# Kernel tuning notes

Measured on AMD Instinct MI355X. Metric: run time of the kernel, lower is better.

## Reference

```python
import jax, jax.numpy as jnp
import numpy as np


def setup_inputs() -> dict:
    key = jax.random.key(0)
    k1, k2, k3 = jax.random.split(key, 3)
    T, B, D, H = 256, 64, 1024, 2048
    sigma = 0.01
    inputs = jax.random.normal(k1, (T, B, D), dtype=jnp.float32)
    state = jnp.zeros((B, H), dtype=jnp.float32)
    W_xh = jax.random.uniform(k2, (D, H), dtype=jnp.float32) * sigma
    W_hh = jax.random.uniform(k3, (H, H), dtype=jnp.float32) * sigma
    b_h = jnp.zeros((H,), dtype=jnp.float32)
    return {"inputs": inputs, "state": state, "W_xh": W_xh, "W_hh": W_hh, "b_h": b_h}


def reference(inputs, state, W_xh, W_hh, b_h):
    # Precompute input projection for all steps in one big GEMM: [T,B,H]
    x_proj = jnp.einsum('tbd,dh->tbh', inputs, W_xh) + b_h

    def step(h, xp):
        h = jnp.tanh(h @ W_hh + xp)
        return h, h

    final_state, outputs = jax.lax.scan(step, state, x_proj)
    # outputs: [T, B, H] (stacked per-step hidden states), final_state: [B, H]
    return outputs, final_state
```

## Files before the change

### kernel.cpp

```cpp
#include <hip/hip_runtime.h>
#include <hip/hip_bf16.h>

#define T_STEPS 256
#define B_SZ    64
#define D_SZ    1024
#define H_SZ    2048
#define NBLK    256
#define TPB     320
#define HBUF    (B_SZ * H_SZ)

#define W_SCALE     256.0f
#define W_INV_SCALE 0.00390625f

typedef __attribute__((ext_vector_type(8))) _Float16 f16x8;
typedef __attribute__((ext_vector_type(4))) _Float16 f16x4;
typedef __attribute__((ext_vector_type(4))) float    f32x4;


__global__ void cvt_f32_f16(const float* __restrict__ in,
                            _Float16* __restrict__ out, int n4, float scale) {
    int i = blockIdx.x * blockDim.x + threadIdx.x;
    if (i < n4) {
        float4 v = ((const float4*)in)[i];
        f16x4 o = { (_Float16)(v.x * scale), (_Float16)(v.y * scale),
                    (_Float16)(v.z * scale), (_Float16)(v.w * scale) };
        ((f16x4*)out)[i] = o;
    }
}

__global__ void transpose_to_f16(const float* __restrict__ in,
                                 _Float16* __restrict__ out,
                                 int rows, int cols, float scale) {
    __shared__ float tile[32][33];
    int tx = threadIdx.x & 31, ty = threadIdx.x >> 5;
    int r0 = blockIdx.y * 32, c0 = blockIdx.x * 32;
#pragma unroll
    for (int i = 0; i < 32; i += 8)
        tile[ty + i][tx] = in[(size_t)(r0 + ty + i) * cols + c0 + tx];
    __syncthreads();
#pragma unroll
    for (int i = 0; i < 32; i += 8)
        out[(size_t)(c0 + ty + i) * rows + r0 + tx] = (_Float16)(tile[tx][ty + i] * scale);
}

__global__ void init_ctrs(unsigned int* ctr) {
    ctr[threadIdx.x + blockIdx.x * blockDim.x] = 0u;
}

#define GBK 32
__device__ __forceinline__ void gload_lds16(const _Float16* g, _Float16* l) {
    __builtin_amdgcn_global_load_lds((const __attribute__((address_space(1))) void*)g,
                                     (__attribute__((address_space(3))) void*)l, 16, 0, 0);
}

__global__ __launch_bounds__(256) void gemm_xproj(
    const _Float16* __restrict__ A,
    const _Float16* __restrict__ BT,
    const float* __restrict__ bias,
    float* __restrict__ C,
    int M, int N, int K)
{
    __shared__ _Float16 As[128 * GBK];
    __shared__ _Float16 Bs[128 * GBK];

    int tid  = threadIdx.x;
    int wave = tid >> 6;
    int lane = tid & 63;
    int q = lane >> 4;
    int r = lane & 15;
    int m0 = blockIdx.x * 128;
    int n0 = blockIdx.y * 128;
    int wr = (wave >> 1) * 64;
    int wc = (wave & 1) * 64;

    int srow  = lane >> 2;
    int skoff = (lane & 3) * 8;

    f32x4 acc[4][4] = {};
    for (int k0 = 0; k0 < K; k0 += GBK) {
#pragma unroll
        for (int i = 0; i < 2; i++) {
            int chunk = wave * 2 + i;
            int row = chunk * 16 + srow;
            gload_lds16(A  + (size_t)(m0 + row) * K + k0 + skoff, As + chunk * 512);
            gload_lds16(BT + (size_t)(n0 + row) * K + k0 + skoff, Bs + chunk * 512);
        }
        __asm__ volatile("s_waitcnt vmcnt(0)" ::: "memory");
        __syncthreads();

        f16x8 a[4], b[4];
#pragma unroll
        for (int i = 0; i < 4; i++)
            a[i] = *(const f16x8*)(As + (wr + i * 16 + r) * GBK + q * 8);
#pragma unroll
        for (int j = 0; j < 4; j++)
            b[j] = *(const f16x8*)(Bs + (wc + j * 16 + r) * GBK + q * 8);
#pragma unroll
        for (int i = 0; i < 4; i++)
#pragma unroll
            for (int j = 0; j < 4; j++)
                acc[i][j] = __builtin_amdgcn_mfma_f32_16x16x32_f16(a[i], b[j], acc[i][j], 0, 0, 0);
        __syncthreads();
    }
#pragma unroll
    for (int i = 0; i < 4; i++)
#pragma unroll
        for (int j = 0; j < 4; j++)
#pragma unroll
            for (int reg = 0; reg < 4; reg++) {
                int row = m0 + wr + i * 16 + q * 4 + reg;
                int col = n0 + wc + j * 16 + r;
                C[(size_t)row * N + col] = acc[i][j][reg] * W_INV_SCALE + bias[col];
            }
}

template<bool CHAIN>
__global__ __launch_bounds__(TPB, 1) void rnn_persist(
    _Float16* __restrict__ hbase,
    _Float16* __restrict__ hb1,
    const _Float16* __restrict__ WT,
    float* __restrict__ out,
    float* __restrict__ final_out,
    unsigned int* __restrict__ ctr)
{
    __shared__ f16x8 wfrag[8192];
    __shared__ float part[4][2][256];
    __shared__ __align__(16) _Float16 hsl[16 * 32];
    __shared__ int pdone[4];
    __shared__ int hdone1, go;

    int tid = threadIdx.x;
    int bid = blockIdx.x;
    int g   = (bid >> 1) & 3;
    int c   = ((bid >> 3) << 1) | (bid & 1);
    int n0  = c * 32;
    int row0 = g * 16;

    if (tid == 0) {
        pdone[0] = pdone[1] = pdone[2] = pdone[3] = 0;
        hdone1 = 0; go = 0;
    }

    for (int idx = tid; idx < 8192; idx += TPB) {
        int kb = idx >> 7, j = (idx >> 6) & 1, l = idx & 63;
        wfrag[idx] = *(const f16x8*)(WT + (size_t)(n0 + j * 16 + (l & 15)) * H_SZ
                                        + kb * 32 + (l >> 4) * 8);
    }
    __syncthreads();

    int wave = tid >> 6, lane = tid & 63;

    if (wave == 4) {
        float c0 = 1.0f + lane, c1 = 2.0f, c2 = 3.0f, c3 = 4.0f;
        const float k1 = 1.0000001f, k2 = 1.0e-30f;
        while (__hip_atomic_load(&go, __ATOMIC_RELAXED, __HIP_MEMORY_SCOPE_WORKGROUP) < T_STEPS) {
#pragma unroll
            for (int z = 0; z < 64; z++) {
                c0 = __builtin_fmaf(c0, k1, k2);
                c1 = __builtin_fmaf(c1, k1, k2);
                c2 = __builtin_fmaf(c2, k1, k2);
                c3 = __builtin_fmaf(c3, k1, k2);
            }
        }
        __asm__ volatile("" :: "v"(c0), "v"(c1), "v"(c2), "v"(c3));
        return;
    }

    int q = lane >> 4, r = lane & 15;
    unsigned int* aline = ctr + (g * 2 + (bid & 1)) * 32;

    float xp[4];
    if (wave < 2) {
#pragma unroll
        for (int s = 0; s < 4; s++)
            xp[s] = out[(size_t)(row0 + q + 4 * s) * H_SZ + n0 + wave * 16 + r];
    }

    for (int t = 0; t < T_STEPS; t++) {
        const _Float16* hp;
        _Float16*       hn;
        if constexpr (CHAIN) {
            hp = hbase + (size_t)t * HBUF;
            hn = hbase + (size_t)(t + 1) * HBUF;
        } else {
            hp = (t & 1) ? hb1 : hbase;
            hn = (t & 1) ? hbase : hb1;
        }
        float* out_t = out + (size_t)t * B_SZ * H_SZ;
        int tg = t + 1;

        const _Float16* arow = hp + (size_t)(row0 + r) * H_SZ + q * 8;
        f16x8 abuf[16];
#pragma unroll
        for (int p = 0; p < 16; p++) {
            if constexpr (CHAIN) {
                abuf[p] = *(const f16x8*)(arow + (wave * 16 + p) * 32);
            } else {
                union { unsigned long long u[2]; f16x8 v; } au;
                au.u[0] = __hip_atomic_load((unsigned long long*)(arow + (wave * 16 + p) * 32),
                                            __ATOMIC_RELAXED, __HIP_MEMORY_SCOPE_AGENT);
                au.u[1] = __hip_atomic_load((unsigned long long*)(arow + (wave * 16 + p) * 32) + 1,
                                            __ATOMIC_RELAXED, __HIP_MEMORY_SCOPE_AGENT);
                abuf[p] = au.v;
            }
        }
        f32x4 acc[2] = {};
#pragma unroll
        for (int p = 0; p < 16; p++) {
            int kb = wave * 16 + p;
            acc[0] = __builtin_amdgcn_mfma_f32_16x16x32_f16(abuf[p], wfrag[kb * 128 + lane],      acc[0], 0, 0, 0);
            acc[1] = __builtin_amdgcn_mfma_f32_16x16x32_f16(abuf[p], wfrag[kb * 128 + 64 + lane], acc[1], 0, 0, 0);
        }

#pragma unroll
        for (int h = 0; h < 2; h++)
            *(f32x4*)&part[wave][h][lane * 4] = acc[h];
        __asm__ volatile("s_waitcnt lgkmcnt(0)" ::: "memory");
        if (lane == 0)
            __hip_atomic_store(&pdone[wave], tg, __ATOMIC_RELAXED, __HIP_MEMORY_SCOPE_WORKGROUP);

        if (wave >= 2) {
            if (t == T_STEPS - 1) break;
            while (__hip_atomic_load(&go, __ATOMIC_RELAXED, __HIP_MEMORY_SCOPE_WORKGROUP) < tg) { }
            continue;
        }

        for (int w = 0; w < 4; w++)
            if (w != wave)
                while (__hip_atomic_load(&pdone[w], __ATOMIC_RELAXED, __HIP_MEMORY_SCOPE_WORKGROUP) < tg) { }
        __asm__ volatile("" ::: "memory");

        bool last = (t == T_STEPS - 1);
#pragma unroll
        for (int s = 0; s < 4; s++) {
            int row = q + 4 * s;
            int idx = (s * 16 + r) * 4 + q;
            float sum = part[0][wave][idx] + part[1][wave][idx]
                      + part[2][wave][idx] + part[3][wave][idx];
            float v = tanhf(sum * W_INV_SCALE + xp[s]);
            size_t o = (size_t)(row0 + row) * H_SZ + n0 + wave * 16 + r;
            out_t[o] = v;
            if (last) final_out[o] = v;
            hsl[row * 32 + wave * 16 + r] = (_Float16)v;
        }
        if (last) {
            if (wave == 0 && lane == 0)
                __hip_atomic_store(&go, T_STEPS, __ATOMIC_RELAXED, __HIP_MEMORY_SCOPE_WORKGROUP);
            break;
        }

        const float* out_t1 = out_t + B_SZ * H_SZ;
#pragma unroll
        for (int s = 0; s < 4; s++)
            xp[s] = out_t1[(size_t)(row0 + q + 4 * s) * H_SZ + n0 + wave * 16 + r];

        __asm__ volatile("s_waitcnt lgkmcnt(0)" ::: "memory");
        {
            int rl = lane >> 2, pi = wave * 4 + (lane & 3);
            unsigned long long vv = ((const unsigned long long*)hsl)[rl * 8 + pi];
            __hip_atomic_store((unsigned long long*)(hn + (size_t)(row0 + rl) * H_SZ + n0) + pi,
                               vv, __ATOMIC_RELAXED, __HIP_MEMORY_SCOPE_AGENT);
        }
        __builtin_amdgcn_s_waitcnt(0);

        if (wave == 1) {
            if (lane == 0)
                __hip_atomic_store(&hdone1, tg, __ATOMIC_RELAXED, __HIP_MEMORY_SCOPE_WORKGROUP);
            while (__hip_atomic_load(&go, __ATOMIC_RELAXED, __HIP_MEMORY_SCOPE_WORKGROUP) < tg) { }
            continue;
        }
        while (__hip_atomic_load(&hdone1, __ATOMIC_RELAXED, __HIP_MEMORY_SCOPE_WORKGROUP) < tg) { }
        if (lane == 0)
            __hip_atomic_fetch_add(aline, 1u, __ATOMIC_RELAXED, __HIP_MEMORY_SCOPE_AGENT);
        unsigned int line_tgt = (unsigned int)tg * 32u;
        for (;;) {
            unsigned int v = __hip_atomic_load(ctr + (g * 2 + (lane & 1)) * 32,
                                               __ATOMIC_RELAXED, __HIP_MEMORY_SCOPE_AGENT);
            if (__ballot(v < line_tgt) == 0ull) break;
        }
        if (lane == 0)
            __hip_atomic_store(&go, tg, __ATOMIC_RELAXED, __HIP_MEMORY_SCOPE_WORKGROUP);
    }
}


extern "C" void kernel_launch(void* const* d_in, const int* in_sizes, int n_in,
                              void* d_out, int out_size, void* d_ws, size_t ws_size,
                              hipStream_t stream) {
    const float* inputs = (const float*)d_in[0];
    const float* state  = (const float*)d_in[1];
    const float* W_xh   = (const float*)d_in[2];
    const float* W_hh   = (const float*)d_in[3];
    const float* b_h    = (const float*)d_in[4];
    float* out = (float*)d_out;
    char* ws = (char*)d_ws;

    const size_t MB = 1ull << 20;
    const size_t OFF_WXT   = 0;
    const size_t OFF_WHT   = 4 * MB;
    const size_t OFF_CTR   = 12 * MB;
    const size_t OFF_CHAIN = 12 * MB + 8192;
    const size_t NEED_CHAIN = OFF_CHAIN + (size_t)(T_STEPS + 1) * HBUF * 2;

    const size_t F_IN  = 0;
    const size_t F_WXT = F_IN  + (size_t)T_STEPS * B_SZ * D_SZ * 2;
    const size_t F_WHT = F_WXT + (size_t)H_SZ * D_SZ * 2;
    const size_t F_H0  = F_WHT + (size_t)H_SZ * H_SZ * 2;
    const size_t F_H1  = F_H0  + (size_t)HBUF * 2;
    const size_t F_CTR = F_H1  + (size_t)HBUF * 2;
    const size_t NEED_PP = F_CTR + 4096;

    const int n_in_el = T_STEPS * B_SZ * D_SZ;
    dim3 g1((T_STEPS * B_SZ) / 128, H_SZ / 128);
    float* final_out = out + (size_t)T_STEPS * B_SZ * H_SZ;

    if (ws_size >= NEED_CHAIN) {
        _Float16* WxT    = (_Float16*)(ws + OFF_WXT);
        _Float16* WhT    = (_Float16*)(ws + OFF_WHT);
        unsigned int* ctr = (unsigned int*)(ws + OFF_CTR);
        _Float16* hchain = (_Float16*)(ws + OFF_CHAIN);
        _Float16* inputs_f16 = hchain + HBUF;
        _Float16* hb1 = nullptr;

        cvt_f32_f16<<<(n_in_el / 4 + 255) / 256, 256, 0, stream>>>(inputs, inputs_f16, n_in_el / 4, 1.0f);
        transpose_to_f16<<<dim3(H_SZ / 32, D_SZ / 32), 256, 0, stream>>>(W_xh, WxT, D_SZ, H_SZ, W_SCALE);
        transpose_to_f16<<<dim3(H_SZ / 32, H_SZ / 32), 256, 0, stream>>>(W_hh, WhT, H_SZ, H_SZ, W_SCALE);
        cvt_f32_f16<<<(B_SZ * H_SZ / 4 + 255) / 256, 256, 0, stream>>>(state, hchain, B_SZ * H_SZ / 4, 1.0f);
        init_ctrs<<<4, 256, 0, stream>>>(ctr);

        gemm_xproj<<<g1, 256, 0, stream>>>(inputs_f16, WxT, b_h, out,
                                           T_STEPS * B_SZ, H_SZ, D_SZ);

        void* args[] = { (void*)&hchain, (void*)&hb1, (void*)&WhT,
                         (void*)&out, (void*)&final_out, (void*)&ctr };
        hipLaunchCooperativeKernel((void*)rnn_persist<true>, dim3(NBLK), dim3(TPB),
                                   args, 0, stream);
    } else {
        if (ws_size < NEED_PP) return;
        _Float16* inputs_f16 = (_Float16*)(ws + F_IN);
        _Float16* WxT    = (_Float16*)(ws + F_WXT);
        _Float16* WhT    = (_Float16*)(ws + F_WHT);
        _Float16* hbuf0  = (_Float16*)(ws + F_H0);
        _Float16* hbuf1  = (_Float16*)(ws + F_H1);
        unsigned int* ctr = (unsigned int*)(ws + F_CTR);

        cvt_f32_f16<<<(n_in_el / 4 + 255) / 256, 256, 0, stream>>>(inputs, inputs_f16, n_in_el / 4, 1.0f);
        transpose_to_f16<<<dim3(H_SZ / 32, D_SZ / 32), 256, 0, stream>>>(W_xh, WxT, D_SZ, H_SZ, W_SCALE);
        transpose_to_f16<<<dim3(H_SZ / 32, H_SZ / 32), 256, 0, stream>>>(W_hh, WhT, H_SZ, H_SZ, W_SCALE);
        cvt_f32_f16<<<(B_SZ * H_SZ / 4 + 255) / 256, 256, 0, stream>>>(state, hbuf0, B_SZ * H_SZ / 4, 1.0f);
        init_ctrs<<<4, 256, 0, stream>>>(ctr);

        gemm_xproj<<<g1, 256, 0, stream>>>(inputs_f16, WxT, b_h, out,
                                           T_STEPS * B_SZ, H_SZ, D_SZ);

        void* args[] = { (void*)&hbuf0, (void*)&hbuf1, (void*)&WhT,
                         (void*)&out, (void*)&final_out, (void*)&ctr };
        hipLaunchCooperativeKernel((void*)rnn_persist<false>, dim3(NBLK), dim3(TPB),
                                   args, 0, stream);
    }
}
```

Baseline: 1.654 ms.

## Replace group barrier with per-block step flags and fuse prep kernels

Replaces the per-step counter barrier across the 64 blocks of a batch group with per-block step flags. Each block publishes its own step count, and each consumer wave polls only the flags of the producer blocks whose columns it reads, so the global barrier and the 'go' broadcast are gone. A local pread handshake stops waves from overwriting the partial sums before they have been consumed. The five preprocessing launches are also merged into one prep_all kernel to save launch overhead. The risk is more flag polling traffic and subtle ordering bugs in the relaxed-memory handshake.

```diff
diff --git a/kernel.cpp b/kernel.cpp
--- a/kernel.cpp
+++ b/kernel.cpp
@@ -16,24 +16,17 @@
 typedef __attribute__((ext_vector_type(4))) _Float16 f16x4;
 typedef __attribute__((ext_vector_type(4))) float    f32x4;
 
-
-__global__ void cvt_f32_f16(const float* __restrict__ in,
-                            _Float16* __restrict__ out, int n4, float scale) {
-    int i = blockIdx.x * blockDim.x + threadIdx.x;
-    if (i < n4) {
-        float4 v = ((const float4*)in)[i];
-        f16x4 o = { (_Float16)(v.x * scale), (_Float16)(v.y * scale),
-                    (_Float16)(v.z * scale), (_Float16)(v.w * scale) };
-        ((f16x4*)out)[i] = o;
-    }
-}
-
-__global__ void transpose_to_f16(const float* __restrict__ in,
-                                 _Float16* __restrict__ out,
-                                 int rows, int cols, float scale) {
-    __shared__ float tile[32][33];
+#define PREP_NI   16384
+#define PREP_NTX  (64 * 32)
+#define PREP_NTH  (64 * 64)
+#define PREP_NS   128
+#define PREP_TOT  (PREP_NI + PREP_NTX + PREP_NTH + PREP_NS + 1)
+
+__device__ __forceinline__ void tile_transpose(
+    const float* __restrict__ in, _Float16* __restrict__ out,
+    int rows, int cols, int bx, int by, float scale, float (*tile)[33]) {
     int tx = threadIdx.x & 31, ty = threadIdx.x >> 5;
-    int r0 = blockIdx.y * 32, c0 = blockIdx.x * 32;
+    int r0 = by * 32, c0 = bx * 32;
 #pragma unroll
     for (int i = 0; i < 32; i += 8)
         tile[ty + i][tx] = in[(size_t)(r0 + ty + i) * cols + c0 + tx];
@@ -43,8 +36,34 @@
         out[(size_t)(c0 + ty + i) * rows + r0 + tx] = (_Float16)(tile[tx][ty + i] * scale);
 }
 
-__global__ void init_ctrs(unsigned int* ctr) {
-    ctr[threadIdx.x + blockIdx.x * blockDim.x] = 0u;
+__global__ void prep_all(const float* __restrict__ inputs, _Float16* __restrict__ xin,
+                         const float* __restrict__ W_xh, _Float16* __restrict__ WxT,
+                         const float* __restrict__ W_hh, _Float16* __restrict__ WhT,
+                         const float* __restrict__ state, _Float16* __restrict__ h0,
+                         unsigned int* __restrict__ ctr) {
+    __shared__ float tile[32][33];
+    int bid = blockIdx.x, tid = threadIdx.x;
+    if (bid < PREP_NI) {
+        int i = bid * 256 + tid;
+        float4 v = ((const float4*)inputs)[i];
+        f16x4 o = { (_Float16)v.x, (_Float16)v.y, (_Float16)v.z, (_Float16)v.w };
+        ((f16x4*)xin)[i] = o;
+    } else if (bid < PREP_NI + PREP_NTX) {
+        int rel = bid - PREP_NI;
+        tile_transpose(W_xh, WxT, D_SZ, H_SZ, rel % 64, rel / 64, W_SCALE, tile);
+    } else if (bid < PREP_NI + PREP_NTX + PREP_NTH) {
+        int rel = bid - PREP_NI - PREP_NTX;
+        tile_transpose(W_hh, WhT, H_SZ, H_SZ, rel % 64, rel / 64, W_SCALE, tile);
+    } else if (bid < PREP_NI + PREP_NTX + PREP_NTH + PREP_NS) {
+        int rel = bid - PREP_NI - PREP_NTX - PREP_NTH;
+        int i = rel * 256 + tid;
+        float4 v = ((const float4*)state)[i];
+        f16x4 o = { (_Float16)v.x, (_Float16)v.y, (_Float16)v.z, (_Float16)v.w };
+        ((f16x4*)h0)[i] = o;
+    } else {
+#pragma unroll
+        for (int k = 0; k < 4; k++) ctr[k * 256 + tid] = 0u;
+    }
 }
 
 #define GBK 32
@@ -127,6 +146,7 @@
     __shared__ float part[4][2][256];
     __shared__ __align__(16) _Float16 hsl[16 * 32];
     __shared__ int pdone[4];
+    __shared__ int pread[2];
     __shared__ int hdone1, go;
 
     int tid = threadIdx.x;
@@ -138,6 +158,7 @@
 
     if (tid == 0) {
         pdone[0] = pdone[1] = pdone[2] = pdone[3] = 0;
+        pread[0] = pread[1] = 0;
         hdone1 = 0; go = 0;
     }
 
@@ -167,7 +188,9 @@
     }
 
     int q = lane >> 4, r = lane & 15;
-    unsigned int* aline = ctr + (g * 2 + (bid & 1)) * 32;
+    unsigned int* flags = ctr + g * 64;
+    unsigned int* myflag = flags + c;
+    unsigned int* pflag  = flags + wave * 16 + (lane & 15);
 
     float xp[4];
     if (wave < 2) {
@@ -188,6 +211,16 @@
         }
         float* out_t = out + (size_t)t * B_SZ * H_SZ;
         int tg = t + 1;
+
+        if (t > 0) {
+            unsigned int need = (unsigned int)t;
+            for (;;) {
+                unsigned int v = __hip_atomic_load(pflag, __ATOMIC_RELAXED,
+                                                   __HIP_MEMORY_SCOPE_AGENT);
+                if (__ballot(v < need) == 0ull) break;
+            }
+            __asm__ volatile("" ::: "memory");
+        }
 
         const _Float16* arow = hp + (size_t)(row0 + r) * H_SZ + q * 8;
         f16x8 abuf[16];
@@ -212,6 +245,12 @@
             acc[1] = __builtin_amdgcn_mfma_f32_16x16x32_f16(abuf[p], wfrag[kb * 128 + 64 + lane], acc[1], 0, 0, 0);
         }
 
+        if (t > 0) {
+            while (__hip_atomic_load(&pread[0], __ATOMIC_RELAXED, __HIP_MEMORY_SCOPE_WORKGROUP) < t ||
+                   __hip_atomic_load(&pread[1], __ATOMIC_RELAXED, __HIP_MEMORY_SCOPE_WORKGROUP) < t) { }
+            __asm__ volatile("" ::: "memory");
+        }
+
 #pragma unroll
         for (int h = 0; h < 2; h++)
             *(f32x4*)&part[wave][h][lane * 4] = acc[h];
@@ -221,7 +260,6 @@
 
         if (wave >= 2) {
             if (t == T_STEPS - 1) break;
-            while (__hip_atomic_load(&go, __ATOMIC_RELAXED, __HIP_MEMORY_SCOPE_WORKGROUP) < tg) { }
             continue;
         }
 
@@ -231,13 +269,20 @@
         __asm__ volatile("" ::: "memory");
 
         bool last = (t == T_STEPS - 1);
+        float sums[4];
+#pragma unroll
+        for (int s = 0; s < 4; s++) {
+            int idx = (s * 16 + r) * 4 + q;
+            sums[s] = part[0][wave][idx] + part[1][wave][idx]
+                    + part[2][wave][idx] + part[3][wave][idx];
+        }
+        if (lane == 0)
+            __hip_atomic_store(&pread[wave], tg, __ATOMIC_RELAXED, __HIP_MEMORY_SCOPE_WORKGROUP);
+
 #pragma unroll
         for (int s = 0; s < 4; s++) {
             int row = q + 4 * s;
-            int idx = (s * 16 + r) * 4 + q;
-            float sum = part[0][wave][idx] + part[1][wave][idx]
-                      + part[2][wave][idx] + part[3][wave][idx];
-            float v = tanhf(sum * W_INV_SCALE + xp[s]);
+            float v = tanhf(sums[s] * W_INV_SCALE + xp[s]);
             size_t o = (size_t)(row0 + row) * H_SZ + n0 + wave * 16 + r;
             out_t[o] = v;
             if (last) final_out[o] = v;
@@ -266,20 +311,12 @@
         if (wave == 1) {
             if (lane == 0)
                 __hip_atomic_store(&hdone1, tg, __ATOMIC_RELAXED, __HIP_MEMORY_SCOPE_WORKGROUP);
-            while (__hip_atomic_load(&go, __ATOMIC_RELAXED, __HIP_MEMORY_SCOPE_WORKGROUP) < tg) { }
             continue;
         }
         while (__hip_atomic_load(&hdone1, __ATOMIC_RELAXED, __HIP_MEMORY_SCOPE_WORKGROUP) < tg) { }
         if (lane == 0)
-            __hip_atomic_fetch_add(aline, 1u, __ATOMIC_RELAXED, __HIP_MEMORY_SCOPE_AGENT);
-        unsigned int line_tgt = (unsigned int)tg * 32u;
-        for (;;) {
-            unsigned int v = __hip_atomic_load(ctr + (g * 2 + (lane & 1)) * 32,
-                                               __ATOMIC_RELAXED, __HIP_MEMORY_SCOPE_AGENT);
-            if (__ballot(v < line_tgt) == 0ull) break;
-        }
-        if (lane == 0)
-            __hip_atomic_store(&go, tg, __ATOMIC_RELAXED, __HIP_MEMORY_SCOPE_WORKGROUP);
+            __hip_atomic_store(myflag, (unsigned int)tg, __ATOMIC_RELAXED,
+                               __HIP_MEMORY_SCOPE_AGENT);
     }
 }
 
@@ -310,7 +347,6 @@
     const size_t F_CTR = F_H1  + (size_t)HBUF * 2;
     const size_t NEED_PP = F_CTR + 4096;
 
-    const int n_in_el = T_STEPS * B_SZ * D_SZ;
     dim3 g1((T_STEPS * B_SZ) / 128, H_SZ / 128);
     float* final_out = out + (size_t)T_STEPS * B_SZ * H_SZ;
 
@@ -322,11 +358,8 @@
         _Float16* inputs_f16 = hchain + HBUF;
         _Float16* hb1 = nullptr;
 
-        cvt_f32_f16<<<(n_in_el / 4 + 255) / 256, 256, 0, stream>>>(inputs, inputs_f16, n_in_el / 4, 1.0f);
-        transpose_to_f16<<<dim3(H_SZ / 32, D_SZ / 32), 256, 0, stream>>>(W_xh, WxT, D_SZ, H_SZ, W_SCALE);
-        transpose_to_f16<<<dim3(H_SZ / 32, H_SZ / 32), 256, 0, stream>>>(W_hh, WhT, H_SZ, H_SZ, W_SCALE);
-        cvt_f32_f16<<<(B_SZ * H_SZ / 4 + 255) / 256, 256, 0, stream>>>(state, hchain, B_SZ * H_SZ / 4, 1.0f);
-        init_ctrs<<<4, 256, 0, stream>>>(ctr);
+        prep_all<<<PREP_TOT, 256, 0, stream>>>(inputs, inputs_f16, W_xh, WxT,
+                                               W_hh, WhT, state, hchain, ctr);
 
         gemm_xproj<<<g1, 256, 0, stream>>>(inputs_f16, WxT, b_h, out,
                                            T_STEPS * B_SZ, H_SZ, D_SZ);
@@ -344,11 +377,8 @@
         _Float16* hbuf1  = (_Float16*)(ws + F_H1);
         unsigned int* ctr = (unsigned int*)(ws + F_CTR);
 
-        cvt_f32_f16<<<(n_in_el / 4 + 255) / 256, 256, 0, stream>>>(inputs, inputs_f16, n_in_el / 4, 1.0f);
-        transpose_to_f16<<<dim3(H_SZ / 32, D_SZ / 32), 256, 0, stream>>>(W_xh, WxT, D_SZ, H_SZ, W_SCALE);
-        transpose_to_f16<<<dim3(H_SZ / 32, H_SZ / 32), 256, 0, stream>>>(W_hh, WhT, H_SZ, H_SZ, W_SCALE);
-        cvt_f32_f16<<<(B_SZ * H_SZ / 4 + 255) / 256, 256, 0, stream>>>(state, hbuf0, B_SZ * H_SZ / 4, 1.0f);
-        init_ctrs<<<4, 256, 0, stream>>>(ctr);
+        prep_all<<<PREP_TOT, 256, 0, stream>>>(inputs, inputs_f16, W_xh, WxT,
+                                               W_hh, WhT, state, hbuf0, ctr);
 
         gemm_xproj<<<g1, 256, 0, stream>>>(inputs_f16, WxT, b_h, out,
                                            T_STEPS * B_SZ, H_SZ, D_SZ);
```

New measurement: 2.345 ms. 41.8% more time.
